# Kernel tuning notes

Measured on AMD Instinct MI355X. Metric: run time of the kernel, lower is better.

## Reference

```python
import jax, jax.numpy as jnp
import numpy as np

H = 16
D_MODEL = 1024
D_K = D_MODEL // H
MAX_REL = 16
REL_VOCAB = 2 * MAX_REL + 1


def _rel_pos_ids(seq_len):
    r = jnp.arange(seq_len)
    dist = r[None, :] - r[:, None]                      # [S,S]
    return jnp.clip(dist, -MAX_REL, MAX_REL) + MAX_REL  # in [0, 2*MAX_REL]


def setup_inputs() -> dict:
    key = jax.random.key(0)
    ks = jax.random.split(key, 16)
    B, S = 2, 2048
    f32 = jnp.float32
    inp = {
        "query": jax.random.normal(ks[0], (B, S, D_MODEL), f32),
        "key": jax.random.normal(ks[1], (B, S, D_MODEL), f32),
        "value": jax.random.normal(ks[2], (B, S, D_MODEL), f32),
        # four nn.Linear(d_model, d_model): W [out,in], b [out]
        "Wq": jax.random.normal(ks[3], (D_MODEL, D_MODEL), f32) * 0.02,
        "bq": jnp.zeros((D_MODEL,), f32),
        "Wk": jax.random.normal(ks[4], (D_MODEL, D_MODEL), f32) * 0.02,
        "bk": jnp.zeros((D_MODEL,), f32),
        "Wv": jax.random.normal(ks[5], (D_MODEL, D_MODEL), f32) * 0.02,
        "bv": jnp.zeros((D_MODEL,), f32),
        "Wo": jax.random.normal(ks[6], (D_MODEL, D_MODEL), f32) * 0.02,
        "bo": jnp.zeros((D_MODEL,), f32),
        # relative-position embedding tables (keys and values)
        "rel_k_table": jax.random.normal(ks[7], (REL_VOCAB, D_K), f32) * 0.02,
        "rel_v_table": jax.random.normal(ks[8], (REL_VOCAB, D_K), f32) * 0.02,
    }
    return inp


def reference(query, key, value, Wq, bq, Wk, bk, Wv, bv, Wo, bo,
              rel_k_table, rel_v_table):
    B, S, E = query.shape
    ids = _rel_pos_ids(S)                    # [S,S] int
    rel_k = rel_k_table[ids]                 # [S,S,d_k]
    rel_v = rel_v_table[ids]                 # [S,S,d_k]

    def proj(x, W, b):
        y = x @ W.T + b                      # [B,S,E]
        return y.reshape(B, S, H, D_K).transpose(0, 2, 1, 3)  # [B,H,S,d_k]

    q = proj(query, Wq, bq)
    k = proj(key, Wk, bk)
    v = proj(value, Wv, bv)

    # NOTE: original has no 1/sqrt(d_k) scaling and ignores mask — faithful.
    logits = jnp.einsum('bhqd,bhkd->bhqk', q, k) \
           + jnp.einsum('bhqd,qkd->bhqk', q, rel_k)
    w = jax.nn.softmax(logits, axis=-1)      # [B,H,S,S]

    x = jnp.einsum('bhqk,bhkd->bhqd', w, v) \
      + jnp.einsum('bhqk,qkd->bhqd', w, rel_v)

    x = x.transpose(0, 2, 1, 3).reshape(B, S, H * D_K)
    return x @ Wo.T + bo
```

## Files before the change

### kernel.cpp

```cpp
#include <hip/hip_runtime.h>
#include <hip/hip_bf16.h>

typedef unsigned short u16;
typedef __attribute__((ext_vector_type(8))) short short8;
typedef __attribute__((ext_vector_type(4))) short short4_t;
typedef __attribute__((ext_vector_type(4))) float f32x4;

#define MFMA16(a, b, c) __builtin_amdgcn_mfma_f32_16x16x32_bf16((a), (b), (c), 0, 0, 0)

#if __has_builtin(__builtin_amdgcn_mfma_f32_16x16x16bf16_1k)
#define MFMAK16(a, b, c) __builtin_amdgcn_mfma_f32_16x16x16bf16_1k((a), (b), (c), 0, 0, 0)
#elif __has_builtin(__builtin_amdgcn_mfma_f32_16x16x16_bf16)
#define MFMAK16(a, b, c) __builtin_amdgcn_mfma_f32_16x16x16_bf16((a), (b), (c), 0, 0, 0)
#else
__device__ __forceinline__ f32x4 mfmak16_asm(short4_t a, short4_t b, f32x4 c) {
  asm("v_mfma_f32_16x16x16_bf16 %0, %1, %2, %0" : "+v"(c) : "v"(a), "v"(b));
  return c;
}
#define MFMAK16(a, b, c) mfmak16_asm((a), (b), (c))
#endif

#define GLOAD_LDS16(gp, lp)                                          \
  __builtin_amdgcn_global_load_lds(                                  \
      (const __attribute__((address_space(1))) void*)(gp),           \
      (__attribute__((address_space(3))) void*)(lp), 16, 0, 0)
#define SBAR() asm volatile("s_barrier" ::: "memory")
#define WAIT_LGKM0() asm volatile("s_waitcnt lgkmcnt(0)" ::: "memory")
#define WAIT_VM0() asm volatile("s_waitcnt vmcnt(0)" ::: "memory")

#define LOG2E 1.44269504088896340736f

__device__ __forceinline__ float us2f(u16 u) {
  union { unsigned int i; float f; } c; c.i = ((unsigned int)u) << 16; return c.f;
}
__device__ __forceinline__ u16 f2us(float f) {
  union { float f; unsigned int i; } c; c.f = f;
  return (u16)((c.i + 0x7fffu + ((c.i >> 16) & 1u)) >> 16);
}
__device__ __forceinline__ unsigned int f2us2(float a, float b) {
  union { __hip_bfloat162 h; unsigned int u; } c;
  c.h = __float22bfloat162_rn(float2{a, b});
  return c.u;
}
__device__ __forceinline__ float exp2fast(float x) {
#if __has_builtin(__builtin_amdgcn_exp2f)
  return __builtin_amdgcn_exp2f(x);
#else
  return exp2f(x);
#endif
}

__global__ __launch_bounds__(256) void cvt_all_kernel(
    const float* x0, const float* x1, const float* x2, const float* w0,
    const float* w1, const float* w2, const float* w3, const float* relk,
    u16* y0, u16* y1, u16* y2, u16* z0, u16* z1, u16* z2, u16* z3,
    u16* relkb) {
  const int z = blockIdx.z;
  if (z == 7) {
    const int i = (blockIdx.x * 256 + threadIdx.x) * 8;
    if (i < 4096) {
      if (i < 2112) {
        const float4 a = *(const float4*)(relk + i);
        const float4 b = *(const float4*)(relk + i + 4);
        unsigned int o[4];
        o[0] = f2us2(a.x, a.y); o[1] = f2us2(a.z, a.w);
        o[2] = f2us2(b.x, b.y); o[3] = f2us2(b.z, b.w);
        *(uint4*)(relkb + i) = *(uint4*)o;
      } else {
        uint4 zz = {0u, 0u, 0u, 0u};
        *(uint4*)(relkb + i) = zz;
      }
    }
    return;
  }
  const float* src; u16* dst; int n;
  switch (z) {
    case 0: src = x0; dst = y0; n = 4194304; break;
    case 1: src = x1; dst = y1; n = 4194304; break;
    case 2: src = x2; dst = y2; n = 4194304; break;
    case 3: src = w0; dst = z0; n = 1048576; break;
    case 4: src = w1; dst = z1; n = 1048576; break;
    case 5: src = w2; dst = z2; n = 1048576; break;
    default: src = w3; dst = z3; n = 1048576; break;
  }
  const int i = (blockIdx.x * 256 + threadIdx.x) * 8;
  if (i < n) {
    const float4 a = *(const float4*)(src + i);
    const float4 b = *(const float4*)(src + i + 4);
    unsigned int o[4];
    o[0] = f2us2(a.x, a.y); o[1] = f2us2(a.z, a.w);
    o[2] = f2us2(b.x, b.y); o[3] = f2us2(b.z, b.w);
    *(uint4*)(dst + i) = *(uint4*)o;
  }
}

template <int MODE, typename OUT, int BM, int BN>
__device__ __forceinline__ void gemm_body(u16* __restrict__ SM,
                                          const u16* __restrict__ X,
                                          const u16* __restrict__ W,
                                          const float* __restrict__ bias,
                                          OUT* __restrict__ Y, int row0, int col0,
                                          float oscale) {
  constexpr int TM = BM / 32, TN = BN / 32;
  u16* As = SM;
  u16* Bs = SM + BM * 64;
  const int tid = threadIdx.x;
  const int lane = tid & 63;
  const int wid = tid >> 6;
  const int wm = wid >> 1, wn = wid & 1;
  const int l15 = lane & 15, l16 = lane >> 4;
  const int lrow = lane >> 3;
  const int lchunk = (lane & 7) ^ lrow;

  f32x4 acc[TM][TN];
#pragma unroll
  for (int i = 0; i < TM; i++)
#pragma unroll
    for (int j = 0; j < TN; j++) acc[i][j] = (f32x4){0.f, 0.f, 0.f, 0.f};

  for (int k0 = 0; k0 < 1024; k0 += 64) {
#pragma unroll
    for (int i = 0; i < TM; i++) {
      const int rb = (wid * TM + i) * 8;
      GLOAD_LDS16(X + (size_t)(row0 + rb + lrow) * 1024 + k0 + lchunk * 8, &As[rb * 64]);
    }
#pragma unroll
    for (int i = 0; i < TN; i++) {
      const int rb = (wid * TN + i) * 8;
      GLOAD_LDS16(W + (size_t)(col0 + rb + lrow) * 1024 + k0 + lchunk * 8, &Bs[rb * 64]);
    }
    __syncthreads();
#pragma unroll
    for (int kk = 0; kk < 2; kk++) {
      const int ch = kk * 4 + l16;
      short8 af[TM], bfr[TN];
#pragma unroll
      for (int t = 0; t < TM; t++) {
        const int m = wm * (BM / 2) + t * 16 + l15;
        af[t] = *(const short8*)&As[m * 64 + ((ch ^ (m & 7)) * 8)];
      }
#pragma unroll
      for (int t = 0; t < TN; t++) {
        const int n = wn * (BN / 2) + t * 16 + l15;
        bfr[t] = *(const short8*)&Bs[n * 64 + ((ch ^ (n & 7)) * 8)];
      }
#pragma unroll
      for (int tm = 0; tm < TM; tm++)
#pragma unroll
        for (int tn = 0; tn < TN; tn++)
          acc[tm][tn] = MFMA16(af[tm], bfr[tn], acc[tm][tn]);
    }
    __syncthreads();
  }

  if (MODE == 0) {
#pragma unroll
    for (int tn = 0; tn < TN; tn++) {
      const int col = col0 + wn * (BN / 2) + tn * 16 + l15;
      const float bv = bias[col];
#pragma unroll
      for (int tm = 0; tm < TM; tm++) {
        const int rowb = row0 + wm * (BM / 2) + tm * 16 + l16 * 4;
#pragma unroll
        for (int r = 0; r < 4; r++)
          Y[(size_t)(rowb + r) * 1024 + col] = (OUT)(acc[tm][tn][r] + bv);
      }
    }
  } else {
    u16* T = SM;
    const int bb = row0 >> 11;
    const int sbase = row0 & 2047;
#pragma unroll
    for (int pass = 0; pass < 2; pass++) {
      __syncthreads();
      if (wm == pass) {
#pragma unroll
        for (int tn = 0; tn < TN; tn++) {
          const int coll = wn * 64 + tn * 16 + l15;
          const float bv = bias[col0 + coll];
#pragma unroll
          for (int tm = 0; tm < TM; tm++) {
            if (MODE == 1) {
#pragma unroll
              for (int r = 0; r < 4; r++)
                T[(tm * 16 + l16 * 4 + r) * 136 + coll] = f2us((acc[tm][tn][r] + bv) * oscale);
            } else {
              unsigned int o[2];
              o[0] = f2us2(acc[tm][tn][0] + bv, acc[tm][tn][1] + bv);
              o[1] = f2us2(acc[tm][tn][2] + bv, acc[tm][tn][3] + bv);
              *(short4_t*)&T[coll * 72 + tm * 16 + l16 * 4] = *(short4_t*)o;
            }
          }
        }
      }
      __syncthreads();
      if (MODE == 1) {
#pragma unroll
        for (int i = 0; i < 8; i++) {
          const int idx = tid + i * 256;
          const int srow = idx >> 5, c4 = idx & 31;
          const short4_t v = *(const short4_t*)&T[srow * 136 + c4 * 4];
          const int col = col0 + c4 * 4;
          const int hh = col >> 6, dd = col & 63;
          const int s = sbase + pass * 64 + srow;
          *(short4_t*)&((u16*)Y)[(((size_t)(bb * 16 + hh)) * 2048 + s) * 64 + dd] = v;
        }
      } else {
#pragma unroll
        for (int i = 0; i < 4; i++) {
          const int idx = tid + i * 256;
          const int cl = idx >> 3, sc = idx & 7;
          const short8 v = *(const short8*)&T[cl * 72 + sc * 8];
          const int col = col0 + cl;
          const int hh = col >> 6, dd = col & 63;
          const int s = sbase + pass * 64 + sc * 8;
          *(short8*)&((u16*)Y)[(((size_t)(bb * 16 + hh)) * 64 + dd) * 2048 + s] = v;
        }
      }
    }
  }
}

__global__ __launch_bounds__(256) void qkv_kernel(
    const u16* Xq, const u16* Xk, const u16* Xv, const u16* Wq, const u16* Wk,
    const u16* Wv, const float* bq, const float* bk, const float* bv, u16* Yq,
    u16* Yk, u16* Yv) {
  __shared__ __align__(16) u16 SM[16384];
  const int z = blockIdx.z;
  const u16* X = z == 0 ? Xq : (z == 1 ? Xk : Xv);
  const u16* W = z == 0 ? Wq : (z == 1 ? Wk : Wv);
  const float* bi = z == 0 ? bq : (z == 1 ? bk : bv);
  u16* Y = z == 0 ? Yq : (z == 1 ? Yk : Yv);
  if (z == 2)
    gemm_body<2, u16, 128, 128>(SM, X, W, bi, Y, blockIdx.x * 128, blockIdx.y * 128, 1.0f);
  else
    gemm_body<1, u16, 128, 128>(SM, X, W, bi, Y, blockIdx.x * 128, blockIdx.y * 128,
                                z == 0 ? LOG2E : 1.0f);
}

__global__ __launch_bounds__(256) void oproj_kernel(const u16* Xc, const u16* Wo,
                                                    const float* bo, float* out) {
  __shared__ __align__(16) u16 SM[8192];
  gemm_body<0, float, 64, 64>(SM, Xc, Wo, bo, out, blockIdx.x * 64, blockIdx.y * 64, 1.0f);
}

__global__ __launch_bounds__(256, 6) void attn_kernel(
    const u16* __restrict__ Qg, const u16* __restrict__ Kg,
    const u16* __restrict__ Vtg, const u16* __restrict__ relkb,
    const float* __restrict__ relv, u16* __restrict__ ctx) {
  __shared__ __align__(16) u16 KV[8192];
  __shared__ __align__(16) u16 qrelJ[64 * 33];
  __shared__ __align__(16) u16 wsum[64 * 32];

  const int tid = threadIdx.x, lane = tid & 63, wid = tid >> 6;
  const int l15 = lane & 15, l16 = lane >> 4;
  const int bh = blockIdx.x;
  const int b = bh >> 4, h = bh & 15;
  const int by = blockIdx.y;
  const int q0 = by * 64;
  const u16* Qb = Qg + (size_t)bh * 2048 * 64;
  const u16* Kb = Kg + (size_t)bh * 2048 * 64;
  const u16* Vtb = Vtg + (size_t)bh * 64 * 2048;

  const int lrow = lane >> 3;
  const int lchunk = (lane & 7) ^ lrow;
  const int qw = wid * 16;
  const int kq4 = l16 * 4;
  const int qrow = qw + l15;

#pragma unroll
  for (int i = 0; i < 2; i++) {
    const int rb = qw + i * 8;
    GLOAD_LDS16(Qb + (size_t)(q0 + rb + lrow) * 64 + lchunk * 8, &KV[rb * 64]);
  }
  for (int idx = tid; idx < 1024; idx += 256) ((unsigned int*)wsum)[idx] = 0u;
  __syncthreads();

  short8 aq[2];
  {
    const int m = qw + l15;
    aq[0] = *(const short8*)&KV[m * 64 + ((l16 ^ (m & 7)) * 8)];
    aq[1] = *(const short8*)&KV[m * 64 + (((4 + l16) ^ (m & 7)) * 8)];
  }
  {
    f32x4 qa[3];
#pragma unroll
    for (int nt = 0; nt < 3; nt++) {
      qa[nt] = (f32x4){0.f, 0.f, 0.f, 0.f};
#pragma unroll
      for (int kk = 0; kk < 2; kk++) {
        const short8 bf =
            *(const short8*)(relkb + (nt * 16 + l15) * 64 + kk * 32 + l16 * 8);
        qa[nt] = MFMA16(aq[kk], bf, qa[nt]);
      }
    }
#pragma unroll
    for (int nt = 0; nt < 3; nt++) {
      if (nt < 2 || l15 == 0) {
#pragma unroll
        for (int r = 0; r < 4; r++)
          qrelJ[(qw + kq4 + r) * 33 + nt * 16 + l15] = f2us(qa[nt][r]);
      }
    }
  }
  WAIT_LGKM0();
  const float q0r = us2f(qrelJ[qrow * 33 + 0]);
  const float q32r = us2f(qrelJ[qrow * 33 + 32]);
  const f32x4 ebl = (f32x4){q0r, q0r, q0r, q0r};
  const f32x4 ebr = (f32x4){q32r, q32r, q32r, q32r};
  const f32x4 zf = (f32x4){0.f, 0.f, 0.f, 0.f};
  const short4_t ones4 = (short4_t){(short)0x3F80, (short)0x3F80,
                                    (short)0x3F80, (short)0x3F80};

  float wl_p = 0.f, wr_p = 0.f;
  f32x4 SL = zf, SR = zf, SD = zf;
  f32x4 Oacc[4];
#pragma unroll
  for (int t = 0; t < 4; t++) Oacc[t] = zf;

  auto stage = [&](int k0c) {
    SBAR();
#pragma unroll
    for (int i = 0; i < 2; i++) {
      const int rb = qw + i * 8;
      GLOAD_LDS16(Kb + (size_t)(k0c + rb + lrow) * 64 + lchunk * 8, &KV[rb * 64]);
    }
#pragma unroll
    for (int i = 0; i < 2; i++) {
      const int rb = qw + i * 8;
      GLOAD_LDS16(Vtb + (size_t)(rb + lrow) * 2048 + k0c + lchunk * 8,
                  &KV[4096 + rb * 64]);
    }
    WAIT_VM0();
    SBAR();
  };

  auto qk = [&](int tn, f32x4 cin) -> f32x4 {
    const int n = tn * 16 + l15;
    const short8 bk0 = *(const short8*)&KV[n * 64 + ((l16 ^ (n & 7)) * 8)];
    const short8 bk1 = *(const short8*)&KV[n * 64 + (((4 + l16) ^ (n & 7)) * 8)];
    f32x4 s = MFMA16(bk0, aq[0], cin);
    s = MFMA16(bk1, aq[1], s);
    return s;
  };

  auto pvstep = [&](const short4_t* pf) {
    __builtin_amdgcn_s_setprio(1);
#pragma unroll
    for (int td = 0; td < 4; td++) {
      const int row = td * 16 + l15;
      const int rs = row & 7;
#pragma unroll
      for (int kk = 0; kk < 4; kk++) {
        const short4_t vf = *(const short4_t*)&KV[4096 + row * 64 +
                                                  (((kk * 2 + (l16 >> 1)) ^ rs) * 8) +
                                                  (l16 & 1) * 4];
        Oacc[td] = MFMAK16(vf, pf[kk], Oacc[td]);
      }
    }
    __builtin_amdgcn_s_setprio(0);
  };

  auto psum = [&](const short4_t* pf, f32x4& S) {
#pragma unroll
    for (int kk = 0; kk < 4; kk++) S = MFMAK16(ones4, pf[kk], S);
  };

  auto offdiag = [&](f32x4 ebv, f32x4& S) {
    short4_t pf[4];
#pragma unroll
    for (int tn = 0; tn < 4; tn++) {
      const f32x4 sac = qk(tn, ebv);
      union { unsigned int u[2]; short4_t s; } c;
      c.u[0] = f2us2(exp2fast(sac[0]), exp2fast(sac[1]));
      c.u[1] = f2us2(exp2fast(sac[2]), exp2fast(sac[3]));
      pf[tn] = c.s;
    }
    pvstep(pf);
    psum(pf, S);
  };

  auto diag = [&](int k0) {
    short4_t pf[4];
#pragma unroll
    for (int tn = 0; tn < 4; tn++) {
      const f32x4 sac = qk(tn, zf);
      float pv4[4];
#pragma unroll
      for (int r = 0; r < 4; r++) {
        const int kg = k0 + tn * 16 + kq4 + r;
        const int dlt = kg - (q0 + qrow);
        const int jj = (dlt < -16 ? -16 : (dlt > 16 ? 16 : dlt)) + 16;
        const float p = exp2fast(sac[r] + us2f(qrelJ[qrow * 33 + jj]));
        pv4[r] = p;
        if (dlt <= -16) wl_p += p;
        else if (dlt >= 16) wr_p += p;
        else wsum[qrow * 32 + (dlt + 15)] = f2us(p);
      }
      union { unsigned int u[2]; short4_t s; } c;
      c.u[0] = f2us2(pv4[0], pv4[1]);
      c.u[1] = f2us2(pv4[2], pv4[3]);
      pf[tn] = c.s;
    }
    pvstep(pf);
    psum(pf, SD);
  };

  const int dlo = (by >= 1) ? by - 1 : 0;
  const int dhi = (by + 2 <= 32) ? by + 2 : 32;
  for (int kt = 0; kt < dlo; ++kt) { stage(kt * 64); offdiag(ebl, SL); }
  for (int kt = dlo; kt < dhi; ++kt) { stage(kt * 64); diag(kt * 64); }
  for (int kt = dhi; kt < 32; ++kt) { stage(kt * 64); offdiag(ebr, SR); }

  wl_p += __shfl_xor(wl_p, 16); wl_p += __shfl_xor(wl_p, 32);
  wr_p += __shfl_xor(wr_p, 16); wr_p += __shfl_xor(wr_p, 32);
  const float l_total = SL[0] + SR[0] + SD[0];
  const float linv = 1.f / l_total;
  const float wl = (SL[0] + wl_p) * linv;
  const float wr = (SR[0] + wr_p) * linv;

  {
    short4_t relf[4][2];
#pragma unroll
    for (int td = 0; td < 4; td++)
#pragma unroll
      for (int kk = 0; kk < 2; kk++) {
        const int jb = kk * 16 + l16 * 4 + 1;
        const int d = td * 16 + l15;
        union { unsigned int u[2]; short4_t s; } c;
        c.u[0] = f2us2(relv[(jb + 0) * 64 + d], relv[(jb + 1) * 64 + d]);
        c.u[1] = f2us2(relv[(jb + 2) * 64 + d], relv[(jb + 3) * 64 + d]);
        relf[td][kk] = c.s;
      }
    WAIT_LGKM0();
    short4_t wfrag[2];
#pragma unroll
    for (int kk = 0; kk < 2; kk++)
      wfrag[kk] = *(const short4_t*)&wsum[qrow * 32 + kk * 16 + l16 * 4];
#pragma unroll
    for (int td = 0; td < 4; td++)
#pragma unroll
      for (int kk = 0; kk < 2; kk++)
        Oacc[td] = MFMAK16(relf[td][kk], wfrag[kk], Oacc[td]);
  }

#pragma unroll
  for (int td = 0; td < 4; td++) {
    const f32x4 rv0 = *(const f32x4*)&relv[td * 16 + kq4];
    const f32x4 rv32 = *(const f32x4*)&relv[32 * 64 + td * 16 + kq4];
#pragma unroll
    for (int r = 0; r < 4; r++)
      Oacc[td][r] = Oacc[td][r] * linv + wl * rv0[r] + wr * rv32[r];
  }

  SBAR();
#pragma unroll
  for (int td = 0; td < 4; td++) {
    unsigned int o[2];
    o[0] = f2us2(Oacc[td][0], Oacc[td][1]);
    o[1] = f2us2(Oacc[td][2], Oacc[td][3]);
    *(short4_t*)&KV[qrow * 72 + td * 16 + kq4] = *(short4_t*)o;
  }
  WAIT_LGKM0();
  SBAR();
#pragma unroll
  for (int i = 0; i < 2; i++) {
    const int idx = tid + i * 256;
    const int q = idx >> 3, sc = idx & 7;
    const short8 v = *(const short8*)&KV[q * 72 + sc * 8];
    *(short8*)&ctx[((size_t)b * 2048 + q0 + q) * 1024 + h * 64 + sc * 8] = v;
  }
}

extern "C" void kernel_launch(void* const* d_in, const int* in_sizes, int n_in,
                              void* d_out, int out_size, void* d_ws, size_t ws_size,
                              hipStream_t stream) {
  u16* qb = (u16*)d_ws;
  u16* kb = qb + 4194304;
  u16* vtb = kb + 4194304;
  u16* ctx = vtb + 4194304;
  u16* Xq = ctx + 4194304;
  u16* Xk = Xq + 4194304;
  u16* Xv = Xk + 4194304;
  u16* Wqb = Xv + 4194304;
  u16* Wkb = Wqb + 1048576;
  u16* Wvb = Wkb + 1048576;
  u16* Wob = Wvb + 1048576;
  u16* relkb = Wob + 1048576;

  const float* bq = (const float*)d_in[4];
  const float* bk = (const float*)d_in[6];
  const float* bv = (const float*)d_in[8];
  const float* bo = (const float*)d_in[10];
  const float* relk = (const float*)d_in[11];
  const float* relv = (const float*)d_in[12];

  dim3 blk(256);
  cvt_all_kernel<<<dim3(2048, 1, 8), blk, 0, stream>>>(
      (const float*)d_in[0], (const float*)d_in[1], (const float*)d_in[2],
      (const float*)d_in[3], (const float*)d_in[5], (const float*)d_in[7],
      (const float*)d_in[9], relk, Xq, Xk, Xv, Wqb, Wkb, Wvb, Wob, relkb);
  qkv_kernel<<<dim3(32, 8, 3), blk, 0, stream>>>(Xq, Xk, Xv, Wqb, Wkb, Wvb, bq,
                                                 bk, bv, qb, kb, vtb);
  attn_kernel<<<dim3(32, 32), blk, 0, stream>>>(qb, kb, vtb, relkb, relv, ctx);
  oproj_kernel<<<dim3(64, 16), blk, 0, stream>>>(ctx, Wob, bo, (float*)d_out);
}
```

Measured before the change: 244.3 us.

## Prefetch V tile through registers one iteration ahead with padded LDS layout

The V^T tile is no longer loaded straight into LDS with global_load_lds. Each iteration now loads the next iteration's V slice into registers and writes the current slice from registers into a padded LDS buffer with row stride 68, which replaces the XOR swizzle. The aim is to hide V global-load latency behind compute. However, the stage still issues a full vmcnt wait right after starting the prefetch, so little overlap may happen. The change also adds register pressure and extra LDS store instructions.

```diff
diff --git a/kernel.cpp b/kernel.cpp
--- a/kernel.cpp
+++ b/kernel.cpp
@@ -248,7 +248,7 @@
     const u16* __restrict__ Qg, const u16* __restrict__ Kg,
     const u16* __restrict__ Vtg, const u16* __restrict__ relkb,
     const float* __restrict__ relv, u16* __restrict__ ctx) {
-  __shared__ __align__(16) u16 KV[8192];
+  __shared__ __align__(16) u16 SM[8448];
   __shared__ __align__(16) u16 qrelJ[64 * 33];
   __shared__ __align__(16) u16 wsum[64 * 32];
 
@@ -268,10 +268,25 @@
   const int kq4 = l16 * 4;
   const int qrow = qw + l15;
 
+  u16* Vs = SM + 4096;
+
+  const int vrow_i = lane >> 3;
+  const int vcol = (lane & 7) * 8;
+  short8 vstage[2];
+  auto loadVreg = [&](int k0c) {
+#pragma unroll
+    for (int i = 0; i < 2; i++) {
+      const int row = qw + i * 8 + vrow_i;
+      vstage[i] = *(const short8*)(Vtb + (size_t)row * 2048 + k0c + vcol);
+    }
+  };
+
+  loadVreg(0);
+
 #pragma unroll
   for (int i = 0; i < 2; i++) {
     const int rb = qw + i * 8;
-    GLOAD_LDS16(Qb + (size_t)(q0 + rb + lrow) * 64 + lchunk * 8, &KV[rb * 64]);
+    GLOAD_LDS16(Qb + (size_t)(q0 + rb + lrow) * 64 + lchunk * 8, &SM[rb * 64]);
   }
   for (int idx = tid; idx < 1024; idx += 256) ((unsigned int*)wsum)[idx] = 0u;
   __syncthreads();
@@ -279,8 +294,8 @@
   short8 aq[2];
   {
     const int m = qw + l15;
-    aq[0] = *(const short8*)&KV[m * 64 + ((l16 ^ (m & 7)) * 8)];
-    aq[1] = *(const short8*)&KV[m * 64 + (((4 + l16) ^ (m & 7)) * 8)];
+    aq[0] = *(const short8*)&SM[m * 64 + ((l16 ^ (m & 7)) * 8)];
+    aq[1] = *(const short8*)&SM[m * 64 + (((4 + l16) ^ (m & 7)) * 8)];
   }
   {
     f32x4 qa[3];
@@ -318,27 +333,28 @@
 #pragma unroll
   for (int t = 0; t < 4; t++) Oacc[t] = zf;
 
-  auto stage = [&](int k0c) {
+  auto stage = [&](int k0c, int k0n) {
     SBAR();
 #pragma unroll
     for (int i = 0; i < 2; i++) {
       const int rb = qw + i * 8;
-      GLOAD_LDS16(Kb + (size_t)(k0c + rb + lrow) * 64 + lchunk * 8, &KV[rb * 64]);
+      GLOAD_LDS16(Kb + (size_t)(k0c + rb + lrow) * 64 + lchunk * 8, &SM[rb * 64]);
     }
 #pragma unroll
     for (int i = 0; i < 2; i++) {
-      const int rb = qw + i * 8;
-      GLOAD_LDS16(Vtb + (size_t)(rb + lrow) * 2048 + k0c + lchunk * 8,
-                  &KV[4096 + rb * 64]);
-    }
+      const int row = qw + i * 8 + vrow_i;
+      *(short8*)&Vs[row * 68 + vcol] = vstage[i];
+    }
+    loadVreg(k0n);
     WAIT_VM0();
+    WAIT_LGKM0();
     SBAR();
   };
 
   auto qk = [&](int tn, f32x4 cin) -> f32x4 {
     const int n = tn * 16 + l15;
-    const short8 bk0 = *(const short8*)&KV[n * 64 + ((l16 ^ (n & 7)) * 8)];
-    const short8 bk1 = *(const short8*)&KV[n * 64 + (((4 + l16) ^ (n & 7)) * 8)];
+    const short8 bk0 = *(const short8*)&SM[n * 64 + ((l16 ^ (n & 7)) * 8)];
+    const short8 bk1 = *(const short8*)&SM[n * 64 + (((4 + l16) ^ (n & 7)) * 8)];
     f32x4 s = MFMA16(bk0, aq[0], cin);
     s = MFMA16(bk1, aq[1], s);
     return s;
@@ -349,13 +365,10 @@
 #pragma unroll
     for (int td = 0; td < 4; td++) {
       const int row = td * 16 + l15;
-      const int rs = row & 7;
 #pragma unroll
       for (int kk = 0; kk < 4; kk++) {
-        const short4_t vf = *(const short4_t*)&KV[4096 + row * 64 +
-                                                  (((kk * 2 + (l16 >> 1)) ^ rs) * 8) +
-                                                  (l16 & 1) * 4];
-        Oacc[td] = MFMAK16(vf, pf[kk], Oacc[td]);
+        const short4_t vfr = *(const short4_t*)&Vs[row * 68 + kk * 16 + kq4];
+        Oacc[td] = MFMAK16(vfr, pf[kk], Oacc[td]);
       }
     }
     __builtin_amdgcn_s_setprio(0);
@@ -408,9 +421,21 @@
 
   const int dlo = (by >= 1) ? by - 1 : 0;
   const int dhi = (by + 2 <= 32) ? by + 2 : 32;
-  for (int kt = 0; kt < dlo; ++kt) { stage(kt * 64); offdiag(ebl, SL); }
-  for (int kt = dlo; kt < dhi; ++kt) { stage(kt * 64); diag(kt * 64); }
-  for (int kt = dhi; kt < 32; ++kt) { stage(kt * 64); offdiag(ebr, SR); }
+  for (int kt = 0; kt < dlo; ++kt) {
+    const int k0 = kt * 64;
+    stage(k0, kt < 31 ? k0 + 64 : k0);
+    offdiag(ebl, SL);
+  }
+  for (int kt = dlo; kt < dhi; ++kt) {
+    const int k0 = kt * 64;
+    stage(k0, kt < 31 ? k0 + 64 : k0);
+    diag(k0);
+  }
+  for (int kt = dhi; kt < 32; ++kt) {
+    const int k0 = kt * 64;
+    stage(k0, kt < 31 ? k0 + 64 : k0);
+    offdiag(ebr, SR);
+  }
 
   wl_p += __shfl_xor(wl_p, 16); wl_p += __shfl_xor(wl_p, 32);
   wr_p += __shfl_xor(wr_p, 16); wr_p += __shfl_xor(wr_p, 32);
@@ -459,7 +484,7 @@
     unsigned int o[2];
     o[0] = f2us2(Oacc[td][0], Oacc[td][1]);
     o[1] = f2us2(Oacc[td][2], Oacc[td][3]);
-    *(short4_t*)&KV[qrow * 72 + td * 16 + kq4] = *(short4_t*)o;
+    *(short4_t*)&SM[qrow * 72 + td * 16 + kq4] = *(short4_t*)o;
   }
   WAIT_LGKM0();
   SBAR();
@@ -467,7 +492,7 @@
   for (int i = 0; i < 2; i++) {
     const int idx = tid + i * 256;
     const int q = idx >> 3, sc = idx & 7;
-    const short8 v = *(const short8*)&KV[q * 72 + sc * 8];
+    const short8 v = *(const short8*)&SM[q * 72 + sc * 8];
     *(short8*)&ctx[((size_t)b * 2048 + q0 + q) * 1024 + h * 64 + sc * 8] = v;
   }
 }
```

Result: slower. 269.6 us (+10.4%).

## Fuse fp32-to-bf16 conversion into GEMM and attention operand loads

Applied to the files above, without the earlier changes.

Removes the separate conversion kernel that wrote bf16 copies of the inputs, the weights and the rel_k table. The GEMMs now read fp32 tiles directly, convert them in registers and write them into swizzled LDS, and the attention kernel converts rel_k rows on the fly. This saves a kernel launch and a full read-write pass over about 60 MB of fp32 data. In exchange, the QKV GEMM reads twice the bytes per tile and loses the asynchronous global-to-LDS load path, and the fp32 weights are converted again by every block that reads them.

```diff
diff --git a/kernel.cpp b/kernel.cpp
--- a/kernel.cpp
+++ b/kernel.cpp
@@ -50,54 +50,10 @@
 #endif
 }
 
-__global__ __launch_bounds__(256) void cvt_all_kernel(
-    const float* x0, const float* x1, const float* x2, const float* w0,
-    const float* w1, const float* w2, const float* w3, const float* relk,
-    u16* y0, u16* y1, u16* y2, u16* z0, u16* z1, u16* z2, u16* z3,
-    u16* relkb) {
-  const int z = blockIdx.z;
-  if (z == 7) {
-    const int i = (blockIdx.x * 256 + threadIdx.x) * 8;
-    if (i < 4096) {
-      if (i < 2112) {
-        const float4 a = *(const float4*)(relk + i);
-        const float4 b = *(const float4*)(relk + i + 4);
-        unsigned int o[4];
-        o[0] = f2us2(a.x, a.y); o[1] = f2us2(a.z, a.w);
-        o[2] = f2us2(b.x, b.y); o[3] = f2us2(b.z, b.w);
-        *(uint4*)(relkb + i) = *(uint4*)o;
-      } else {
-        uint4 zz = {0u, 0u, 0u, 0u};
-        *(uint4*)(relkb + i) = zz;
-      }
-    }
-    return;
-  }
-  const float* src; u16* dst; int n;
-  switch (z) {
-    case 0: src = x0; dst = y0; n = 4194304; break;
-    case 1: src = x1; dst = y1; n = 4194304; break;
-    case 2: src = x2; dst = y2; n = 4194304; break;
-    case 3: src = w0; dst = z0; n = 1048576; break;
-    case 4: src = w1; dst = z1; n = 1048576; break;
-    case 5: src = w2; dst = z2; n = 1048576; break;
-    default: src = w3; dst = z3; n = 1048576; break;
-  }
-  const int i = (blockIdx.x * 256 + threadIdx.x) * 8;
-  if (i < n) {
-    const float4 a = *(const float4*)(src + i);
-    const float4 b = *(const float4*)(src + i + 4);
-    unsigned int o[4];
-    o[0] = f2us2(a.x, a.y); o[1] = f2us2(a.z, a.w);
-    o[2] = f2us2(b.x, b.y); o[3] = f2us2(b.z, b.w);
-    *(uint4*)(dst + i) = *(uint4*)o;
-  }
-}
-
-template <int MODE, typename OUT, int BM, int BN>
+template <int MODE, typename OUT, int BM, int BN, bool AF32, bool BF32>
 __device__ __forceinline__ void gemm_body(u16* __restrict__ SM,
-                                          const u16* __restrict__ X,
-                                          const u16* __restrict__ W,
+                                          const void* __restrict__ Xp,
+                                          const void* __restrict__ Wp,
                                           const float* __restrict__ bias,
                                           OUT* __restrict__ Y, int row0, int col0,
                                           float oscale) {
@@ -111,6 +67,17 @@
   const int l15 = lane & 15, l16 = lane >> 4;
   const int lrow = lane >> 3;
   const int lchunk = (lane & 7) ^ lrow;
+  const int schunk = lane & 7;
+
+  auto stage8f = [&](u16* dst, const float* src, int trow) {
+    const float* p = src + schunk * 8;
+    const float4 a = *(const float4*)p;
+    const float4 b2 = *(const float4*)(p + 4);
+    unsigned int o[4];
+    o[0] = f2us2(a.x, a.y); o[1] = f2us2(a.z, a.w);
+    o[2] = f2us2(b2.x, b2.y); o[3] = f2us2(b2.z, b2.w);
+    *(short8*)&dst[trow * 64 + ((schunk ^ (trow & 7)) * 8)] = *(short8*)o;
+  };
 
   f32x4 acc[TM][TN];
 #pragma unroll
@@ -119,15 +86,35 @@
     for (int j = 0; j < TN; j++) acc[i][j] = (f32x4){0.f, 0.f, 0.f, 0.f};
 
   for (int k0 = 0; k0 < 1024; k0 += 64) {
-#pragma unroll
-    for (int i = 0; i < TM; i++) {
-      const int rb = (wid * TM + i) * 8;
-      GLOAD_LDS16(X + (size_t)(row0 + rb + lrow) * 1024 + k0 + lchunk * 8, &As[rb * 64]);
-    }
-#pragma unroll
-    for (int i = 0; i < TN; i++) {
-      const int rb = (wid * TN + i) * 8;
-      GLOAD_LDS16(W + (size_t)(col0 + rb + lrow) * 1024 + k0 + lchunk * 8, &Bs[rb * 64]);
+    if constexpr (AF32) {
+      const float* X = (const float*)Xp;
+#pragma unroll
+      for (int i = 0; i < TM; i++) {
+        const int rb = (wid * TM + i) * 8 + lrow;
+        stage8f(As, X + (size_t)(row0 + rb) * 1024 + k0, rb);
+      }
+    } else {
+      const u16* X = (const u16*)Xp;
+#pragma unroll
+      for (int i = 0; i < TM; i++) {
+        const int rb = (wid * TM + i) * 8;
+        GLOAD_LDS16(X + (size_t)(row0 + rb + lrow) * 1024 + k0 + lchunk * 8, &As[rb * 64]);
+      }
+    }
+    if constexpr (BF32) {
+      const float* W = (const float*)Wp;
+#pragma unroll
+      for (int i = 0; i < TN; i++) {
+        const int rb = (wid * TN + i) * 8 + lrow;
+        stage8f(Bs, W + (size_t)(col0 + rb) * 1024 + k0, rb);
+      }
+    } else {
+      const u16* W = (const u16*)Wp;
+#pragma unroll
+      for (int i = 0; i < TN; i++) {
+        const int rb = (wid * TN + i) * 8;
+        GLOAD_LDS16(W + (size_t)(col0 + rb + lrow) * 1024 + k0 + lchunk * 8, &Bs[rb * 64]);
+      }
     }
     __syncthreads();
 #pragma unroll
@@ -222,31 +209,34 @@
 }
 
 __global__ __launch_bounds__(256) void qkv_kernel(
-    const u16* Xq, const u16* Xk, const u16* Xv, const u16* Wq, const u16* Wk,
-    const u16* Wv, const float* bq, const float* bk, const float* bv, u16* Yq,
-    u16* Yk, u16* Yv) {
+    const float* Xq, const float* Xk, const float* Xv, const float* Wq,
+    const float* Wk, const float* Wv, const float* bq, const float* bk,
+    const float* bv, u16* Yq, u16* Yk, u16* Yv) {
   __shared__ __align__(16) u16 SM[16384];
   const int z = blockIdx.z;
-  const u16* X = z == 0 ? Xq : (z == 1 ? Xk : Xv);
-  const u16* W = z == 0 ? Wq : (z == 1 ? Wk : Wv);
+  const float* X = z == 0 ? Xq : (z == 1 ? Xk : Xv);
+  const float* W = z == 0 ? Wq : (z == 1 ? Wk : Wv);
   const float* bi = z == 0 ? bq : (z == 1 ? bk : bv);
   u16* Y = z == 0 ? Yq : (z == 1 ? Yk : Yv);
   if (z == 2)
-    gemm_body<2, u16, 128, 128>(SM, X, W, bi, Y, blockIdx.x * 128, blockIdx.y * 128, 1.0f);
+    gemm_body<2, u16, 128, 128, true, true>(SM, X, W, bi, Y, blockIdx.x * 128,
+                                            blockIdx.y * 128, 1.0f);
   else
-    gemm_body<1, u16, 128, 128>(SM, X, W, bi, Y, blockIdx.x * 128, blockIdx.y * 128,
-                                z == 0 ? LOG2E : 1.0f);
-}
-
-__global__ __launch_bounds__(256) void oproj_kernel(const u16* Xc, const u16* Wo,
+    gemm_body<1, u16, 128, 128, true, true>(SM, X, W, bi, Y, blockIdx.x * 128,
+                                            blockIdx.y * 128,
+                                            z == 0 ? LOG2E : 1.0f);
+}
+
+__global__ __launch_bounds__(256) void oproj_kernel(const u16* Xc, const float* Wo,
                                                     const float* bo, float* out) {
   __shared__ __align__(16) u16 SM[8192];
-  gemm_body<0, float, 64, 64>(SM, Xc, Wo, bo, out, blockIdx.x * 64, blockIdx.y * 64, 1.0f);
+  gemm_body<0, float, 64, 64, false, true>(SM, Xc, Wo, bo, out, blockIdx.x * 64,
+                                           blockIdx.y * 64, 1.0f);
 }
 
 __global__ __launch_bounds__(256, 6) void attn_kernel(
     const u16* __restrict__ Qg, const u16* __restrict__ Kg,
-    const u16* __restrict__ Vtg, const u16* __restrict__ relkb,
+    const u16* __restrict__ Vtg, const float* __restrict__ relk,
     const float* __restrict__ relv, u16* __restrict__ ctx) {
   __shared__ __align__(16) u16 KV[8192];
   __shared__ __align__(16) u16 qrelJ[64 * 33];
@@ -289,8 +279,19 @@
       qa[nt] = (f32x4){0.f, 0.f, 0.f, 0.f};
 #pragma unroll
       for (int kk = 0; kk < 2; kk++) {
-        const short8 bf =
-            *(const short8*)(relkb + (nt * 16 + l15) * 64 + kk * 32 + l16 * 8);
+        const int rr = nt * 16 + l15;
+        short8 bf;
+        if (rr < 33) {
+          const float* p = relk + rr * 64 + kk * 32 + l16 * 8;
+          const float4 a = *(const float4*)p;
+          const float4 b2 = *(const float4*)(p + 4);
+          unsigned int o[4];
+          o[0] = f2us2(a.x, a.y); o[1] = f2us2(a.z, a.w);
+          o[2] = f2us2(b2.x, b2.y); o[3] = f2us2(b2.z, b2.w);
+          bf = *(short8*)o;
+        } else {
+          bf = (short8){0, 0, 0, 0, 0, 0, 0, 0};
+        }
         qa[nt] = MFMA16(aq[kk], bf, qa[nt]);
       }
     }
@@ -479,29 +480,24 @@
   u16* kb = qb + 4194304;
   u16* vtb = kb + 4194304;
   u16* ctx = vtb + 4194304;
-  u16* Xq = ctx + 4194304;
-  u16* Xk = Xq + 4194304;
-  u16* Xv = Xk + 4194304;
-  u16* Wqb = Xv + 4194304;
-  u16* Wkb = Wqb + 1048576;
-  u16* Wvb = Wkb + 1048576;
-  u16* Wob = Wvb + 1048576;
-  u16* relkb = Wob + 1048576;
-
+
+  const float* query = (const float*)d_in[0];
+  const float* key = (const float*)d_in[1];
+  const float* value = (const float*)d_in[2];
+  const float* Wq = (const float*)d_in[3];
   const float* bq = (const float*)d_in[4];
+  const float* Wk = (const float*)d_in[5];
   const float* bk = (const float*)d_in[6];
+  const float* Wv = (const float*)d_in[7];
   const float* bv = (const float*)d_in[8];
+  const float* Wo = (const float*)d_in[9];
   const float* bo = (const float*)d_in[10];
   const float* relk = (const float*)d_in[11];
   const float* relv = (const float*)d_in[12];
 
   dim3 blk(256);
-  cvt_all_kernel<<<dim3(2048, 1, 8), blk, 0, stream>>>(
-      (const float*)d_in[0], (const float*)d_in[1], (const float*)d_in[2],
-      (const float*)d_in[3], (const float*)d_in[5], (const float*)d_in[7],
-      (const float*)d_in[9], relk, Xq, Xk, Xv, Wqb, Wkb, Wvb, Wob, relkb);
-  qkv_kernel<<<dim3(32, 8, 3), blk, 0, stream>>>(Xq, Xk, Xv, Wqb, Wkb, Wvb, bq,
-                                                 bk, bv, qb, kb, vtb);
-  attn_kernel<<<dim3(32, 32), blk, 0, stream>>>(qb, kb, vtb, relkb, relv, ctx);
-  oproj_kernel<<<dim3(64, 16), blk, 0, stream>>>(ctx, Wob, bo, (float*)d_out);
-}
+  qkv_kernel<<<dim3(32, 8, 3), blk, 0, stream>>>(query, key, value, Wq, Wk, Wv,
+                                                 bq, bk, bv, qb, kb, vtb);
+  attn_kernel<<<dim3(32, 32), blk, 0, stream>>>(qb, kb, vtb, relk, relv, ctx);
+  oproj_kernel<<<dim3(64, 16), blk, 0, stream>>>(ctx, Wo, bo, (float*)d_out);
+}
```

Measured after the change: 279.3 us. +14.3%, slower.
